# Kernel tuning notes

Measured on AMD Instinct MI355X. Metric: run time of the kernel, lower is better.

Reference implementation:

```python
import jax, jax.numpy as jnp
import numpy as np

D, H, N, BS = 3072, 2048, 16, 512
MAX_LATENT_VAR = 0.1


def setup_inputs() -> dict:
    key = jax.random.key(0)
    ks = jax.random.split(key, 12)
    s = 0.02
    return {
        "x": jax.random.normal(ks[0], (BS, D), dtype=jnp.float32),
        "eps": jax.random.normal(ks[1], (1, BS, N), dtype=jnp.float32),
        "enc_W1": jax.random.normal(ks[2], (D, H), dtype=jnp.float32) * s,
        "enc_b1": jnp.zeros((H,), dtype=jnp.float32),
        "enc_Wmu": jax.random.normal(ks[3], (H, N), dtype=jnp.float32) * s,
        "enc_bmu": jnp.zeros((N,), dtype=jnp.float32),
        "enc_Wls": jax.random.normal(ks[4], (H, 1), dtype=jnp.float32) * s,
        "enc_bls": jnp.zeros((1,), dtype=jnp.float32),
        "dec_W1": jax.random.normal(ks[5], (N, H), dtype=jnp.float32) * 0.1,
        "dec_b1": jnp.zeros((H,), dtype=jnp.float32),
        "dec_W2": jax.random.normal(ks[6], (H, D), dtype=jnp.float32) * s,
        "dec_b2": jnp.zeros((D,), dtype=jnp.float32),
    }


def reference(x, eps, enc_W1, enc_b1, enc_Wmu, enc_bmu, enc_Wls, enc_bls,
              dec_W1, dec_b1, dec_W2, dec_b2):
    bs, Dd = x.shape
    n = dec_W1.shape[0]

    def dec(z):  # smooth 2-layer MLP decoder (supports nested autodiff)
        return jnp.tanh(z @ dec_W1 + dec_b1) @ dec_W2 + dec_b2

    # encoder.forward_with_sigma
    h = jnp.tanh(x @ enc_W1 + enc_b1)
    z_star = h @ enc_Wmu + enc_bmu                      # (bs, n)
    sigma = jnp.exp(h @ enc_Wls + enc_bls)[:, 0]        # (bs,)

    # per-sample Jacobian of decoder: (bs, D, n)
    J = jax.vmap(jax.jacfwd(dec))(z_star)

    # per-sample Hessian of f(z) = stop_grad(d) . d,  d = (x - dec(z)) / sigma
    def f_hess(z, xi, sg):
        d = (xi - dec(z)) / sg
        return jnp.dot(jax.lax.stop_gradient(d), d)
    hess = jax.vmap(jax.hessian(f_hess), in_axes=(0, 0, 0))(z_star, x, sigma)  # (bs,n,n)

    eye = jnp.eye(n, dtype=x.dtype)
    Prec = jnp.einsum('bdi,bdj->bij', J, J) / (sigma ** 2)[:, None, None] + eye + hess

    eigvals = jnp.linalg.eigvalsh(Prec)                 # ascending, (bs, n)
    eigmin = eigvals[:, 0]
    delta = 1.0 / MAX_LATENT_VAR - eigmin               # (bs,)
    Prec = Prec + eye * delta[:, None, None]
    eigvals = eigvals + delta[:, None]

    # upper-triangular Cholesky: U^T U = Prec
    U = jnp.swapaxes(jnp.linalg.cholesky(Prec), -1, -2)  # (bs, n, n)

    def solve1(u, e):  # solve U y = e
        return jax.scipy.linalg.solve_triangular(u, e[:, None], lower=False)[:, 0]
    z_off = jax.vmap(jax.vmap(solve1, in_axes=(0, 0)), in_axes=(None, 0))(U, eps)  # (ne,bs,n)
    z_sample = z_star[None] + z_off

    n_eval = eps.shape[0]
    recon = dec(z_sample.reshape(-1, n)).reshape(n_eval, bs, Dd)
    recon_loss = ((recon - x[None]) ** 2).sum(axis=2).mean(axis=0) / (2.0 * sigma ** 2)
    latent_energy = (z_star ** 2).sum(axis=1) / 2.0 + (1.0 / eigvals).sum(axis=1) / 2.0
    logdet_loss = jnp.log(eigvals).sum(axis=1) / 2.0
    sigma_loss = Dd * jnp.log(sigma)
    neg_log_prob = (recon_loss + latent_energy + logdet_loss + sigma_loss) / Dd
    return (neg_log_prob, recon_loss, latent_energy, logdet_loss, sigma)
```

## Files before the change

### kernel.cpp

```cpp
#include <hip/hip_runtime.h>
#include <hip/hip_bf16.h>
#include <math.h>

#define D_ 3072
#define H_ 2048
#define N_ 16
#define BS_ 512

typedef short s16x8 __attribute__((ext_vector_type(8)));
typedef float f32x4v __attribute__((ext_vector_type(4)));
typedef __hip_bfloat16 bf16;

__device__ __forceinline__ void gload_lds16(const void* g, void* l) {
    __builtin_amdgcn_global_load_lds((const __attribute__((address_space(1))) void*)g,
                                     (__attribute__((address_space(3))) void*)l, 16, 0, 0);
}

__device__ __forceinline__ float bf2f(unsigned short u) {
    unsigned v = (unsigned)u << 16; float f; __builtin_memcpy(&f, &v, 4); return f;
}

__global__ __launch_bounds__(256) void mfma_nt_sk(
    const bf16* __restrict__ A, const bf16* __restrict__ Bt,
    float* __restrict__ C, int M, int N, int K, int KC)
{
    __shared__ __align__(16) bf16 As[128 * 32];
    __shared__ __align__(16) bf16 Bs[128 * 32];
    const int tid = threadIdx.x;
    const int w = tid >> 6, l = tid & 63;
    const int wr = w >> 1, wc = w & 1;
    const int m0 = blockIdx.y * 128, n0 = blockIdx.x * 128;
    const int kbeg = blockIdx.z * KC;

    f32x4v acc[4][4];
    #pragma unroll
    for (int a = 0; a < 4; ++a)
        #pragma unroll
        for (int b = 0; b < 4; ++b) acc[a][b] = (f32x4v){0.f, 0.f, 0.f, 0.f};

    const int srow = l >> 2;
    const int scol = (l & 3) * 8;

    for (int k0 = kbeg; k0 < kbeg + KC; k0 += 32) {
        #pragma unroll
        for (int q = 0; q < 2; ++q) {
            int r0 = w * 32 + q * 16;
            gload_lds16(&A[(size_t)(m0 + r0 + srow) * K + k0 + scol], &As[r0 * 32]);
            gload_lds16(&Bt[(size_t)(n0 + r0 + srow) * K + k0 + scol], &Bs[r0 * 32]);
        }
        __syncthreads();
        s16x8 af[4], bfr[4];
        #pragma unroll
        for (int mf = 0; mf < 4; ++mf)
            af[mf] = *(const s16x8*)&As[(wr * 64 + mf * 16 + (l & 15)) * 32 + (l >> 4) * 8];
        #pragma unroll
        for (int nf = 0; nf < 4; ++nf)
            bfr[nf] = *(const s16x8*)&Bs[(wc * 64 + nf * 16 + (l & 15)) * 32 + (l >> 4) * 8];
        #pragma unroll
        for (int mf = 0; mf < 4; ++mf)
            #pragma unroll
            for (int nf = 0; nf < 4; ++nf)
                acc[mf][nf] = __builtin_amdgcn_mfma_f32_16x16x32_bf16(af[mf], bfr[nf], acc[mf][nf], 0, 0, 0);
        __syncthreads();
    }

    #pragma unroll
    for (int mf = 0; mf < 4; ++mf)
        #pragma unroll
        for (int nf = 0; nf < 4; ++nf) {
            int n = n0 + wc * 64 + nf * 16 + (l & 15);
            #pragma unroll
            for (int r = 0; r < 4; ++r) {
                int m = m0 + wr * 64 + mf * 16 + (l >> 4) * 4 + r;
                atomicAdd(&C[(size_t)m * N + n], acc[mf][nf][r]);
            }
        }
}

__global__ __launch_bounds__(256) void ep_ebf(const float* __restrict__ C,
    const float* __restrict__ bias, const float* __restrict__ X,
    bf16* __restrict__ Eout, int MN, int N)
{
    int base = (blockIdx.x * 256 + threadIdx.x) * 8;
    if (base < MN) {
        float4 c0 = *(const float4*)&C[base];
        float4 c1 = *(const float4*)&C[base + 4];
        float4 x0 = *(const float4*)&X[base];
        float4 x1 = *(const float4*)&X[base + 4];
        int n = base % N;
        float4 b0 = *(const float4*)&bias[n];
        float4 b1 = *(const float4*)&bias[n + 4];
        union { s16x8 v; bf16 e[8]; } u;
        u.e[0] = __float2bfloat16(x0.x - (c0.x + b0.x));
        u.e[1] = __float2bfloat16(x0.y - (c0.y + b0.y));
        u.e[2] = __float2bfloat16(x0.z - (c0.z + b0.z));
        u.e[3] = __float2bfloat16(x0.w - (c0.w + b0.w));
        u.e[4] = __float2bfloat16(x1.x - (c1.x + b1.x));
        u.e[5] = __float2bfloat16(x1.y - (c1.y + b1.y));
        u.e[6] = __float2bfloat16(x1.z - (c1.z + b1.z));
        u.e[7] = __float2bfloat16(x1.w - (c1.w + b1.w));
        *(s16x8*)&Eout[base] = u.v;
    }
}

__global__ __launch_bounds__(256) void ep_recon(const float* __restrict__ C,
    const float* __restrict__ bias, const float* __restrict__ X, float* __restrict__ rls)
{
    int m = blockIdx.x;
    float s = 0.f;
    for (int n = threadIdx.x * 4; n < D_; n += 1024) {
        float4 c = *(const float4*)&C[(size_t)m * D_ + n];
        float4 bb = *(const float4*)&bias[n];
        float4 xx = *(const float4*)&X[(size_t)m * D_ + n];
        float v0 = c.x + bb.x - xx.x, v1 = c.y + bb.y - xx.y;
        float v2 = c.z + bb.z - xx.z, v3 = c.w + bb.w - xx.w;
        s += v0 * v0 + v1 * v1 + v2 * v2 + v3 * v3;
    }
    __shared__ float red[4];
    int wid = threadIdx.x >> 6, lane = threadIdx.x & 63;
    #pragma unroll
    for (int off = 32; off; off >>= 1) s += __shfl_xor(s, off);
    if (lane == 0) red[wid] = s;
    __syncthreads();
    if (threadIdx.x == 0) rls[m] = red[0] + red[1] + red[2] + red[3];
}

__global__ __launch_bounds__(256) void jtj_fused(
    const bf16* __restrict__ Vt, const bf16* __restrict__ W2t,
    float* __restrict__ S, int Mb, int b0)
{
    __shared__ union {
        struct { __align__(16) bf16 As[128 * 32]; __align__(16) bf16 Bs[128 * 32]; } s;
        __align__(16) bf16 J[128 * 136];
    } u;
    const int tid = threadIdx.x;
    const int w = tid >> 6, l = tid & 63;
    const int wr = w >> 1, wc = w & 1;

    int mb, nb;
    if ((Mb & 7) == 0) {
        int lin = blockIdx.y * 24 + blockIdx.x;
        int xcd = lin & 7, idx = lin >> 3;
        int mchunk = Mb >> 3;
        mb = xcd * mchunk + idx / 24;
        nb = idx % 24;
    } else { mb = blockIdx.y; nb = blockIdx.x; }
    const int m0 = mb * 128, n0 = nb * 128;

    f32x4v acc[4][4];
    #pragma unroll
    for (int a = 0; a < 4; ++a)
        #pragma unroll
        for (int b = 0; b < 4; ++b) acc[a][b] = (f32x4v){0.f, 0.f, 0.f, 0.f};

    const int srow = l >> 2;
    const int scol = (l & 3) * 8;

    for (int k0 = 0; k0 < H_; k0 += 32) {
        #pragma unroll
        for (int q = 0; q < 2; ++q) {
            int r0 = w * 32 + q * 16;
            gload_lds16(&Vt[(size_t)(m0 + r0 + srow) * H_ + k0 + scol], &u.s.As[r0 * 32]);
            gload_lds16(&W2t[(size_t)(n0 + r0 + srow) * H_ + k0 + scol], &u.s.Bs[r0 * 32]);
        }
        __syncthreads();
        s16x8 af[4], bfr[4];
        #pragma unroll
        for (int mf = 0; mf < 4; ++mf)
            af[mf] = *(const s16x8*)&u.s.As[(wr * 64 + mf * 16 + (l & 15)) * 32 + (l >> 4) * 8];
        #pragma unroll
        for (int nf = 0; nf < 4; ++nf)
            bfr[nf] = *(const s16x8*)&u.s.Bs[(wc * 64 + nf * 16 + (l & 15)) * 32 + (l >> 4) * 8];
        #pragma unroll
        for (int mf = 0; mf < 4; ++mf)
            #pragma unroll
            for (int nf = 0; nf < 4; ++nf)
                acc[mf][nf] = __builtin_amdgcn_mfma_f32_16x16x32_bf16(af[mf], bfr[nf], acc[mf][nf], 0, 0, 0);
        __syncthreads();
    }

    __syncthreads();
    #pragma unroll
    for (int mf = 0; mf < 4; ++mf) {
        int rbase = wr * 64 + mf * 16 + (l >> 4) * 4;
        #pragma unroll
        for (int nf = 0; nf < 4; ++nf) {
            int col = wc * 64 + nf * 16 + (l & 15);
            #pragma unroll
            for (int r = 0; r < 4; ++r)
                u.J[(rbase + r) * 136 + col] = __float2bfloat16(acc[mf][nf][r]);
        }
    }
    __syncthreads();

    #pragma unroll
    for (int t2 = 0; t2 < 2; ++t2) {
        int bl = w * 2 + t2;
        f32x4v sp = (f32x4v){0.f, 0.f, 0.f, 0.f};
        #pragma unroll
        for (int kq = 0; kq < 4; ++kq) {
            s16x8 fr = *(const s16x8*)&u.J[(bl * 16 + (l & 15)) * 136 + kq * 32 + (l >> 4) * 8];
            sp = __builtin_amdgcn_mfma_f32_16x16x32_bf16(fr, fr, sp, 0, 0, 0);
        }
        int bglob = b0 + mb * 8 + bl;
        #pragma unroll
        for (int r = 0; r < 4; ++r)
            atomicAdd(&S[(size_t)bglob * 256 + ((l >> 4) * 4 + r) * 16 + (l & 15)], sp[r]);
    }
}

__global__ __launch_bounds__(256) void hess_mfma(const float* __restrict__ t,
    const float* __restrict__ g, const bf16* __restrict__ W1b, float* __restrict__ S)
{
    const int w = threadIdx.x >> 6, l = threadIdx.x & 63;
    const int b = blockIdx.x * 4 + w;
    const int row = l & 15, kq = (l >> 4) * 8;

    f32x4v sp = (f32x4v){0.f, 0.f, 0.f, 0.f};
    for (int k0 = 0; k0 < H_; k0 += 32) {
        int kk = k0 + kq;
        s16x8 wf = *(const s16x8*)&W1b[(size_t)row * H_ + kk];
        float4 t0 = *(const float4*)&t[(size_t)b * H_ + kk];
        float4 t1 = *(const float4*)&t[(size_t)b * H_ + kk + 4];
        float4 g0 = *(const float4*)&g[(size_t)b * H_ + kk];
        float4 g1 = *(const float4*)&g[(size_t)b * H_ + kk + 4];
        float wv[8];
        wv[0] = 2.f * g0.x * t0.x * (1.f - t0.x * t0.x);
        wv[1] = 2.f * g0.y * t0.y * (1.f - t0.y * t0.y);
        wv[2] = 2.f * g0.z * t0.z * (1.f - t0.z * t0.z);
        wv[3] = 2.f * g0.w * t0.w * (1.f - t0.w * t0.w);
        wv[4] = 2.f * g1.x * t1.x * (1.f - t1.x * t1.x);
        wv[5] = 2.f * g1.y * t1.y * (1.f - t1.y * t1.y);
        wv[6] = 2.f * g1.z * t1.z * (1.f - t1.z * t1.z);
        wv[7] = 2.f * g1.w * t1.w * (1.f - t1.w * t1.w);
        union { s16x8 v; bf16 e[8]; } af;
        #pragma unroll
        for (int e = 0; e < 8; ++e)
            af.e[e] = __float2bfloat16(wv[e] * bf2f((unsigned short)wf[e]));
        sp = __builtin_amdgcn_mfma_f32_16x16x32_bf16(af.v, wf, sp, 0, 0, 0);
    }
    #pragma unroll
    for (int r = 0; r < 4; ++r)
        S[(size_t)b * 256 + ((l >> 4) * 4 + r) * 16 + (l & 15)] += sp[r];
}

__global__ __launch_bounds__(256) void prep_all(
    const float* __restrict__ x, const float* __restrict__ enc_W1,
    const float* __restrict__ dec_W2, const float* __restrict__ dec_W1,
    bf16* __restrict__ x_bf, bf16* __restrict__ eW1t,
    bf16* __restrict__ W2t, bf16* __restrict__ W2b, bf16* __restrict__ W1b)
{
    __shared__ float tile[64][65];
    const int blk = blockIdx.x;
    const int tid = threadIdx.x;
    if (blk < 768) {
        int i = blk * 256 + tid;
        const float4* p = (const float4*)x + (size_t)i * 2;
        float4 a = p[0], b = p[1];
        union { s16x8 v; bf16 e[8]; } u;
        u.e[0] = __float2bfloat16(a.x); u.e[1] = __float2bfloat16(a.y);
        u.e[2] = __float2bfloat16(a.z); u.e[3] = __float2bfloat16(a.w);
        u.e[4] = __float2bfloat16(b.x); u.e[5] = __float2bfloat16(b.y);
        u.e[6] = __float2bfloat16(b.z); u.e[7] = __float2bfloat16(b.w);
        *(s16x8*)&x_bf[(size_t)i * 8] = u.v;
    } else if (blk < 768 + 1536) {
        int bid = blk - 768;
        int r0 = (bid % 48) * 64, c0 = (bid / 48) * 64;
        int tx = tid & 63, ty = tid >> 6;
        #pragma unroll
        for (int k = 0; k < 16; ++k) {
            int rr = ty * 16 + k;
            tile[rr][tx] = enc_W1[(size_t)(r0 + rr) * H_ + c0 + tx];
        }
        __syncthreads();
        #pragma unroll
        for (int k = 0; k < 16; ++k) {
            int cc = ty * 16 + k;
            eW1t[(size_t)(c0 + cc) * D_ + r0 + tx] = __float2bfloat16(tile[tx][cc]);
        }
    } else if (blk < 768 + 3072) {
        int bid = blk - 768 - 1536;
        int r0 = (bid % 32) * 64, c0 = (bid / 32) * 64;
        int tx = tid & 63, ty = tid >> 6;
        #pragma unroll
        for (int k = 0; k < 16; ++k) {
            int rr = ty * 16 + k;
            float v = dec_W2[(size_t)(r0 + rr) * D_ + c0 + tx];
            tile[rr][tx] = v;
            W2b[(size_t)(r0 + rr) * D_ + c0 + tx] = __float2bfloat16(v);
        }
        __syncthreads();
        #pragma unroll
        for (int k = 0; k < 16; ++k) {
            int cc = ty * 16 + k;
            W2t[(size_t)(c0 + cc) * H_ + r0 + tx] = __float2bfloat16(tile[tx][cc]);
        }
    } else {
        int i = (blk - 768 - 3072) * 256 + tid;
        if (i < N_ * H_ / 8) {
            const float4* p = (const float4*)dec_W1 + (size_t)i * 2;
            float4 a = p[0], b = p[1];
            union { s16x8 v; bf16 e[8]; } u;
            u.e[0] = __float2bfloat16(a.x); u.e[1] = __float2bfloat16(a.y);
            u.e[2] = __float2bfloat16(a.z); u.e[3] = __float2bfloat16(a.w);
            u.e[4] = __float2bfloat16(b.x); u.e[5] = __float2bfloat16(b.y);
            u.e[6] = __float2bfloat16(b.z); u.e[7] = __float2bfloat16(b.w);
            *(s16x8*)&W1b[(size_t)i * 8] = u.v;
        }
    }
}

__global__ __launch_bounds__(256) void zsig_t_kernel(const float* __restrict__ Ch,
    const float* __restrict__ enc_b1, const float* __restrict__ Wmu, const float* __restrict__ bmu,
    const float* __restrict__ Wls, const float* __restrict__ bls,
    const float* __restrict__ dW1, const float* __restrict__ db1,
    float* __restrict__ z_star, float* __restrict__ lsig, float* __restrict__ sigma,
    float* __restrict__ t, bf16* __restrict__ tb)
{
    const int b = blockIdx.x, tid = threadIdx.x;
    float acc[17];
    #pragma unroll
    for (int i = 0; i < 17; ++i) acc[i] = 0.f;
    for (int hh = tid; hh < H_; hh += 256) {
        float hv = tanhf(Ch[(size_t)b * H_ + hh] + enc_b1[hh]);
        const float* wr = &Wmu[(size_t)hh * 16];
        #pragma unroll
        for (int i = 0; i < 16; ++i) acc[i] += hv * wr[i];
        acc[16] += hv * Wls[hh];
    }
    __shared__ float red[17][4];
    __shared__ float zs[16];
    const int wid = tid >> 6, lane = tid & 63;
    #pragma unroll
    for (int i = 0; i < 17; ++i) {
        float v = acc[i];
        #pragma unroll
        for (int off = 32; off; off >>= 1) v += __shfl_xor(v, off);
        if (lane == 0) red[i][wid] = v;
    }
    __syncthreads();
    if (tid < 17) {
        float v = red[tid][0] + red[tid][1] + red[tid][2] + red[tid][3];
        if (tid < 16) { float z = v + bmu[tid]; zs[tid] = z; z_star[(size_t)b * 16 + tid] = z; }
        else { float ls = v + bls[0]; lsig[b] = ls; sigma[b] = expf(ls); }
    }
    __syncthreads();
    for (int hh = tid; hh < H_; hh += 256) {
        float a = db1[hh];
        #pragma unroll
        for (int i = 0; i < 16; ++i) a += zs[i] * dW1[(size_t)i * H_ + hh];
        float tv = tanhf(a);
        t[(size_t)b * H_ + hh] = tv;
        tb[(size_t)b * H_ + hh] = __float2bfloat16(tv);
    }
}

__global__ __launch_bounds__(256) void build_t(const float* __restrict__ z,
    const float* __restrict__ W1, const float* __restrict__ b1, bf16* __restrict__ tb)
{
    __shared__ float zs[16];
    int b = blockIdx.x, tid = threadIdx.x;
    if (tid < 16) zs[tid] = z[(size_t)b * 16 + tid];
    __syncthreads();
    for (int hh = tid; hh < H_; hh += 256) {
        float a = b1[hh];
        #pragma unroll
        for (int i = 0; i < 16; ++i) a += zs[i] * W1[(size_t)i * H_ + hh];
        tb[(size_t)b * H_ + hh] = __float2bfloat16(tanhf(a));
    }
}

__global__ __launch_bounds__(256) void build_vt(const float* __restrict__ t,
    const float* __restrict__ W1, bf16* __restrict__ Vt, int b0)
{
    int bl = blockIdx.x, b = b0 + bl, tid = threadIdx.x;
    __shared__ float u[H_];
    for (int hh = tid; hh < H_; hh += 256) {
        float tv = t[(size_t)b * H_ + hh];
        u[hh] = 1.f - tv * tv;
    }
    __syncthreads();
    size_t base = (size_t)bl * 16 * H_;
    int hh = tid * 8;
    for (int i = 0; i < 16; ++i) {
        union { s16x8 v; bf16 e[8]; } pk;
        #pragma unroll
        for (int k = 0; k < 8; ++k)
            pk.e[k] = __float2bfloat16(u[hh + k] * W1[(size_t)i * H_ + hh + k]);
        *(s16x8*)&Vt[base + (size_t)i * H_ + hh] = pk.v;
    }
}

__global__ __launch_bounds__(64) void solve_kernel(const float* __restrict__ S,
    const float* __restrict__ sigma, const float* __restrict__ z_star,
    const float* __restrict__ eps, float* __restrict__ z_sample, float* __restrict__ d_out)
{
    const int lane = threadIdx.x;
    const int q = lane >> 4;
    const int j = lane & 15;
    const int b = blockIdx.x * 4 + q;

    const float sg = sigma[b];
    const float inv_s2 = 1.0f / (sg * sg);

    float a0[16], a[16];
    #pragma unroll
    for (int r = 0; r < 16; ++r) {
        a0[r] = S[(size_t)b * 256 + r * 16 + j] * inv_s2 + ((r == j) ? 1.0f : 0.0f);
        a[r] = a0[r];
    }

    #pragma unroll
    for (int k = 0; k < 14; ++k) {
        float x[16];
        #pragma unroll
        for (int r = 0; r < 16; ++r) x[r] = __shfl(a[k], r, 16);
        float sig2 = 0.f;
        #pragma unroll
        for (int r = 0; r < 16; ++r) if (r > k + 1) sig2 += x[r] * x[r];
        float x0 = x[k + 1];
        float normx = sqrtf(sig2 + x0 * x0);
        float alpha = (x0 >= 0.f) ? -normx : normx;
        float v[16];
        #pragma unroll
        for (int r = 0; r < 16; ++r)
            v[r] = (r <= k) ? 0.f : ((r == k + 1) ? x0 - alpha : x[r]);
        float vtv = 0.f;
        #pragma unroll
        for (int r = 0; r < 16; ++r) vtv += v[r] * v[r];
        float beta = (vtv > 1e-28f) ? 2.0f / vtv : 0.f;
        float sj = 0.f;
        #pragma unroll
        for (int r = 0; r < 16; ++r) sj += a[r] * v[r];
        float av[16];
        #pragma unroll
        for (int r = 0; r < 16; ++r) av[r] = __shfl(sj, r, 16);
        float vtav = 0.f;
        #pragma unroll
        for (int r = 0; r < 16; ++r) vtav += v[r] * av[r];
        float c = 0.5f * beta * vtav;
        float wv[16];
        #pragma unroll
        for (int r = 0; r < 16; ++r) wv[r] = beta * (av[r] - c * v[r]);
        float vj = (j <= k) ? 0.f : ((j == k + 1) ? a[k] - alpha : a[k]);
        float wj = beta * (sj - c * vj);
        #pragma unroll
        for (int r = 0; r < 16; ++r) a[r] -= v[r] * wj + wv[r] * vj;
    }

    float dg[16], eo[15];
    #pragma unroll
    for (int r = 0; r < 16; ++r) dg[r] = __shfl(a[r], r, 16);
    #pragma unroll
    for (int r = 0; r < 15; ++r) eo[r] = __shfl(a[r + 1], r, 16);

    float lo = 1e30f, hi = 1e30f;
    #pragma unroll
    for (int r = 0; r < 16; ++r) {
        float rad = ((r > 0) ? fabsf(eo[r - 1]) : 0.f) + ((r < 15) ? fabsf(eo[r]) : 0.f);
        lo = fminf(lo, dg[r] - rad);
        hi = fminf(hi, dg[r]);
    }
    lo -= 1e-4f; hi += 1e-4f;

    #pragma unroll
    for (int pass = 0; pass < 5; ++pass) {
        float step = (hi - lo) * (1.0f / 17.0f);
        float s = lo + step * (float)(j + 1);
        float qq = dg[0] - s;
        int cnt = (qq < 0.f) ? 1 : 0;
        #pragma unroll
        for (int i = 1; i < 16; ++i) {
            float denom = (fabsf(qq) < 1e-30f) ? -1e-30f : qq;
            qq = dg[i] - s - eo[i - 1] * eo[i - 1] / denom;
            cnt += (qq < 0.f) ? 1 : 0;
        }
        unsigned long long bal = __ballot(cnt >= 1);
        unsigned grp = (unsigned)((bal >> (q * 16)) & 0xffffull);
        int f = grp ? (__ffs(grp) - 1) : 16;
        float nlo = lo + step * (float)f;
        float nhi = (f < 16) ? (lo + step * (float)(f + 1)) : hi;
        lo = nlo; hi = nhi;
    }
    const float lam_min = 0.5f * (lo + hi);
    const float delta = 10.0f - lam_min;

    float bm[16];
    #pragma unroll
    for (int r = 0; r < 16; ++r) bm[r] = a0[r] + ((r == j) ? delta : 0.f);

    float ldsum = 0.f;
    #pragma unroll
    for (int kk = 0; kk < 16; ++kk) {
        float ck[16];
        #pragma unroll
        for (int r = 0; r < 16; ++r) ck[r] = __shfl(bm[kk], r, 16);
        float dkk = sqrtf(fmaxf(ck[kk], 1e-30f));
        float inv = 1.0f / dkk;
        ldsum += logf(dkk);
        float lfull[16];
        #pragma unroll
        for (int r = 0; r < 16; ++r) lfull[r] = ck[r] * inv;
        float lj = bm[kk] * inv;
        if (j == kk) {
            #pragma unroll
            for (int r = 0; r < 16; ++r) bm[r] = (r >= kk) ? lfull[r] : 0.f;
        } else if (j > kk) {
            #pragma unroll
            for (int r = 0; r < 16; ++r)
                if (r > kk) bm[r] -= lfull[r] * lj;
        }
    }

    float w[16];
    #pragma unroll
    for (int r = 0; r < 16; ++r) w[r] = 0.f;
    #pragma unroll
    for (int i = 0; i < 16; ++i) {
        float row[16];
        #pragma unroll
        for (int kx = 0; kx < 16; ++kx) row[kx] = __shfl(bm[i], kx, 16);
        float sacc = 0.f;
        #pragma unroll
        for (int kx = 0; kx < 16; ++kx) if (kx < i) sacc += row[kx] * w[kx];
        float invd = 1.0f / row[i];
        float val = (i == j) ? invd : (-sacc * invd);
        w[i] = (i >= j) ? val : 0.f;
    }

    float tsum = 0.f;
    #pragma unroll
    for (int r = 0; r < 16; ++r) tsum += w[r] * w[r];
    float zv = z_star[(size_t)b * 16 + j];
    float ep = eps[(size_t)b * 16 + j];
    float epsv[16];
    #pragma unroll
    for (int r = 0; r < 16; ++r) epsv[r] = __shfl(ep, r, 16);
    float zoff = 0.f;
    #pragma unroll
    for (int r = 0; r < 16; ++r) zoff += w[r] * epsv[r];
    z_sample[(size_t)b * 16 + j] = zv + zoff;

    float zsq = zv * zv;
    #pragma unroll
    for (int off = 1; off < 16; off <<= 1) {
        tsum += __shfl_xor(tsum, off);
        zsq  += __shfl_xor(zsq, off);
    }
    if (j == 0) {
        d_out[2 * 512 + b] = 0.5f * zsq + 0.5f * tsum;
        d_out[3 * 512 + b] = ldsum;
        d_out[4 * 512 + b] = sg;
    }
}

__global__ void finalize_kernel(const float* __restrict__ rlsum, const float* __restrict__ sigma,
    const float* __restrict__ lsig, float* __restrict__ d_out)
{
    int b = blockIdx.x * 256 + threadIdx.x;
    if (b < BS_) {
        float sg = sigma[b];
        float rl = rlsum[b] / (2.0f * sg * sg);
        float le = d_out[2 * 512 + b];
        float ld = d_out[3 * 512 + b];
        d_out[b] = (rl + le + ld) / 3072.0f + lsig[b];
        d_out[512 + b] = rl;
    }
}

extern "C" void kernel_launch(void* const* d_in, const int* in_sizes, int n_in,
                              void* d_out, int out_size, void* d_ws, size_t ws_size,
                              hipStream_t stream)
{
    const float* x       = (const float*)d_in[0];
    const float* eps     = (const float*)d_in[1];
    const float* enc_W1  = (const float*)d_in[2];
    const float* enc_b1  = (const float*)d_in[3];
    const float* enc_Wmu = (const float*)d_in[4];
    const float* enc_bmu = (const float*)d_in[5];
    const float* enc_Wls = (const float*)d_in[6];
    const float* enc_bls = (const float*)d_in[7];
    const float* dec_W1  = (const float*)d_in[8];
    const float* dec_b1  = (const float*)d_in[9];
    const float* dec_W2  = (const float*)d_in[10];
    const float* dec_b2  = (const float*)d_in[11];
    float* out = (float*)d_out;

    char* wsb = (char*)d_ws;
    size_t off = 0;
    auto alloc = [&](size_t bytes) -> void* {
        off = (off + 255) & ~(size_t)255;
        void* p = wsb + off;
        off += bytes;
        return p;
    };

    float* Ch   = (float*)alloc((size_t)BS_ * H_ * 4);
    float* Cd   = (float*)alloc((size_t)BS_ * D_ * 4);
    float* g    = (float*)alloc((size_t)BS_ * H_ * 4);
    float* S    = (float*)alloc((size_t)BS_ * 256 * 4);
    size_t zero_span = (size_t)((char*)(S + BS_ * 256) - (char*)Ch);

    float* t    = (float*)alloc((size_t)BS_ * H_ * 4);
    float* z_st = (float*)alloc((size_t)BS_ * 16 * 4);
    float* lsig = (float*)alloc(BS_ * 4);
    float* sigm = (float*)alloc(BS_ * 4);
    float* z_sm = (float*)alloc((size_t)BS_ * 16 * 4);
    float* rls  = (float*)alloc(BS_ * 4);
    bf16* x_bf  = (bf16*)alloc((size_t)BS_ * D_ * 2);
    bf16* eW1t  = (bf16*)alloc((size_t)H_ * D_ * 2);
    bf16* W2b   = (bf16*)alloc((size_t)H_ * D_ * 2);
    bf16* W2t   = (bf16*)alloc((size_t)D_ * H_ * 2);
    bf16* W1b   = (bf16*)alloc((size_t)N_ * H_ * 2);
    bf16* t_bf  = (bf16*)alloc((size_t)BS_ * H_ * 2);
    bf16* e_bf  = (bf16*)alloc((size_t)BS_ * D_ * 2);
    bf16* t2b   = (bf16*)alloc((size_t)BS_ * H_ * 2);

    int nb = 0;
    size_t base_off = off;
    const int cand[3] = {512, 128, 32};
    bf16* Vt = nullptr;
    for (int ci = 0; ci < 3; ++ci) {
        off = base_off;
        int n = cand[ci];
        bf16* vt = (bf16*)alloc((size_t)n * 16 * H_ * 2);
        if (off <= ws_size) { nb = n; Vt = vt; break; }
    }
    if (nb == 0) return;

    prep_all<<<dim3(768 + 3072 + 16), 256, 0, stream>>>(
        x, enc_W1, dec_W2, dec_W1, x_bf, eW1t, W2t, W2b, W1b);
    hipMemsetAsync(Ch, 0, zero_span, stream);

    mfma_nt_sk<<<dim3(H_ / 128, BS_ / 128, 4), 256, 0, stream>>>(
        x_bf, eW1t, Ch, BS_, H_, D_, D_ / 4);
    zsig_t_kernel<<<dim3(BS_), 256, 0, stream>>>(Ch, enc_b1, enc_Wmu, enc_bmu, enc_Wls, enc_bls,
        dec_W1, dec_b1, z_st, lsig, sigm, t, t_bf);
    mfma_nt_sk<<<dim3(D_ / 128, BS_ / 128, 4), 256, 0, stream>>>(
        t_bf, W2t, Cd, BS_, D_, H_, H_ / 4);
    ep_ebf<<<dim3(BS_ * D_ / 8 / 256), 256, 0, stream>>>(Cd, dec_b2, x, e_bf, BS_ * D_, D_);
    mfma_nt_sk<<<dim3(H_ / 128, BS_ / 128, 4), 256, 0, stream>>>(
        e_bf, W2b, g, BS_, H_, D_, D_ / 4);

    for (int b0 = 0; b0 < BS_; b0 += nb) {
        build_vt<<<dim3(nb), 256, 0, stream>>>(t, dec_W1, Vt, b0);
        jtj_fused<<<dim3(D_ / 128, nb * 16 / 128), 256, 0, stream>>>(
            Vt, W2t, S, nb * 16 / 128, b0);
    }
    hess_mfma<<<dim3(BS_ / 4), 256, 0, stream>>>(t, g, W1b, S);

    solve_kernel<<<dim3(BS_ / 4), 64, 0, stream>>>(S, sigm, z_st, eps, z_sm, out);
    build_t<<<dim3(BS_), 256, 0, stream>>>(z_sm, dec_W1, dec_b1, t2b);
    hipMemsetAsync(Cd, 0, (size_t)BS_ * D_ * 4, stream);
    mfma_nt_sk<<<dim3(D_ / 128, BS_ / 128, 4), 256, 0, stream>>>(
        t2b, W2t, Cd, BS_, D_, H_, H_ / 4);
    ep_recon<<<dim3(BS_), 256, 0, stream>>>(Cd, dec_b2, x, rls);
    finalize_kernel<<<dim3(2), 256, 0, stream>>>(rls, sigm, lsig, out);
}
```

Before: 359.3 us.

## Rewrite JtJ GEMM as 256x256-tile, 8-wave double-buffered MFMA kernel

Replaces the 128x128 jtj_fused kernel with jtj8: 512-thread blocks computing 256x256 tiles over 64-wide K steps. Shared-memory staging is double-buffered with XOR-swizzled LDS layout, and prefetch is interleaved with the MFMA phases using barriers and setprio. It also uses an XCD-aware block swizzle and a two-pass epilogue that builds the per-sample J^T J. The aim is more data reuse per global load, fewer bank conflicts and overlap of loads with compute. In exchange it needs 128 KB of dynamic LDS with one block per CU, and it assumes nb*16 is a multiple of 256 and the block count a multiple of 8.

Result: slower. 386.2 us (+7.5%).

```diff
diff --git a/kernel.cpp b/kernel.cpp
--- a/kernel.cpp
+++ b/kernel.cpp
@@ -6,6 +6,7 @@
 #define H_ 2048
 #define N_ 16
 #define BS_ 512
+#define NT_ (H_ / 64)
 
 typedef short s16x8 __attribute__((ext_vector_type(8)));
 typedef float f32x4v __attribute__((ext_vector_type(4)));
@@ -125,87 +126,124 @@
     if (threadIdx.x == 0) rls[m] = red[0] + red[1] + red[2] + red[3];
 }
 
-__global__ __launch_bounds__(256) void jtj_fused(
+__global__ __launch_bounds__(512, 1) void jtj8(
     const bf16* __restrict__ Vt, const bf16* __restrict__ W2t,
-    float* __restrict__ S, int Mb, int b0)
-{
-    __shared__ union {
-        struct { __align__(16) bf16 As[128 * 32]; __align__(16) bf16 Bs[128 * 32]; } s;
-        __align__(16) bf16 J[128 * 136];
-    } u;
+    float* __restrict__ S, int nwg, int b0)
+{
+    extern __shared__ __align__(16) char smem[];
+    char* Abase = smem;
+    char* Bbase = smem + 65536;
     const int tid = threadIdx.x;
     const int w = tid >> 6, l = tid & 63;
-    const int wr = w >> 1, wc = w & 1;
-
-    int mb, nb;
-    if ((Mb & 7) == 0) {
-        int lin = blockIdx.y * 24 + blockIdx.x;
-        int xcd = lin & 7, idx = lin >> 3;
-        int mchunk = Mb >> 3;
-        mb = xcd * mchunk + idx / 24;
-        nb = idx % 24;
-    } else { mb = blockIdx.y; nb = blockIdx.x; }
-    const int m0 = mb * 128, n0 = nb * 128;
-
-    f32x4v acc[4][4];
-    #pragma unroll
-    for (int a = 0; a < 4; ++a)
-        #pragma unroll
-        for (int b = 0; b < 4; ++b) acc[a][b] = (f32x4v){0.f, 0.f, 0.f, 0.f};
-
-    const int srow = l >> 2;
-    const int scol = (l & 3) * 8;
-
-    for (int k0 = 0; k0 < H_; k0 += 32) {
-        #pragma unroll
-        for (int q = 0; q < 2; ++q) {
-            int r0 = w * 32 + q * 16;
-            gload_lds16(&Vt[(size_t)(m0 + r0 + srow) * H_ + k0 + scol], &u.s.As[r0 * 32]);
-            gload_lds16(&W2t[(size_t)(n0 + r0 + srow) * H_ + k0 + scol], &u.s.Bs[r0 * 32]);
+    const int wr = w >> 2, wc = w & 3;
+
+    const int bid = blockIdx.x;
+    const int swz = (bid & 7) * (nwg >> 3) + (bid >> 3);
+    const int mb = swz / 12, nbk = swz % 12;
+    const int m0 = mb * 256, n0 = nbk * 256;
+
+    const int srow = tid >> 3;
+    const int sswz = (((tid & 7) ^ ((tid >> 3) & 7)) << 4);
+
+    f32x4v acc[8][4];
+    #pragma unroll
+    for (int i = 0; i < 8; ++i)
+        #pragma unroll
+        for (int j = 0; j < 4; ++j) acc[i][j] = (f32x4v){0.f, 0.f, 0.f, 0.f};
+
+    auto STAGE = [&](int u, int t, int bi) {
+        const char* gsrc;
+        char* ldst;
+        if (u < 2) {
+            gsrc = (const char*)Vt + ((size_t)(m0 + u * 128 + srow) * H_ + t * 64) * 2 + sswz;
+            ldst = Abase + bi * 32768 + u * 16384 + w * 1024;
+        } else {
+            gsrc = (const char*)W2t + ((size_t)(n0 + (u - 2) * 128 + srow) * H_ + t * 64) * 2 + sswz;
+            ldst = Bbase + bi * 32768 + (u - 2) * 16384 + w * 1024;
+        }
+        gload_lds16(gsrc, ldst);
+        gload_lds16(gsrc + (size_t)64 * H_ * 2, ldst + 8192);
+    };
+
+    #pragma unroll
+    for (int u = 0; u < 4; ++u) STAGE(u, 0, 0);
+    asm volatile("s_waitcnt vmcnt(0)" ::: "memory");
+    __builtin_amdgcn_s_barrier();
+    __builtin_amdgcn_sched_barrier(0);
+
+    for (int T = 0; T < NT_; ++T) {
+        const int bi = T & 1;
+        const char* Ab = Abase + bi * 32768;
+        const char* Bb = Bbase + bi * 32768;
+        #pragma unroll
+        for (int p = 0; p < 4; ++p) {
+            const int qa = p >> 1, qb = p & 1;
+            s16x8 af[4][2], bfv[2][2];
+            #pragma unroll
+            for (int i = 0; i < 4; ++i) {
+                int arow = wr * 128 + (qa * 4 + i) * 16 + (l & 15);
+                #pragma unroll
+                for (int kh = 0; kh < 2; ++kh)
+                    af[i][kh] = *(const s16x8*)(Ab + arow * 128 +
+                        ((kh * 64 + (l >> 4) * 16) ^ ((l & 7) << 4)));
+            }
+            #pragma unroll
+            for (int j = 0; j < 2; ++j) {
+                int brow = wc * 64 + (qb * 2 + j) * 16 + (l & 15);
+                #pragma unroll
+                for (int kh = 0; kh < 2; ++kh)
+                    bfv[j][kh] = *(const s16x8*)(Bb + brow * 128 +
+                        ((kh * 64 + (l >> 4) * 16) ^ ((l & 7) << 4)));
+            }
+            if (T + 1 < NT_) STAGE(p, T + 1, bi ^ 1);
+            if (p == 3) asm volatile("s_waitcnt vmcnt(0)" ::: "memory");
+            __builtin_amdgcn_s_barrier();
+            __builtin_amdgcn_sched_barrier(0);
+            __builtin_amdgcn_s_setprio(1);
+            #pragma unroll
+            for (int i = 0; i < 4; ++i)
+                #pragma unroll
+                for (int j = 0; j < 2; ++j) {
+                    acc[qa * 4 + i][qb * 2 + j] = __builtin_amdgcn_mfma_f32_16x16x32_bf16(
+                        af[i][0], bfv[j][0], acc[qa * 4 + i][qb * 2 + j], 0, 0, 0);
+                    acc[qa * 4 + i][qb * 2 + j] = __builtin_amdgcn_mfma_f32_16x16x32_bf16(
+                        af[i][1], bfv[j][1], acc[qa * 4 + i][qb * 2 + j], 0, 0, 0);
+                }
+            __builtin_amdgcn_s_setprio(0);
+            __builtin_amdgcn_s_barrier();
+            __builtin_amdgcn_sched_barrier(0);
+        }
+    }
+
+    __syncthreads();
+    bf16* Jl = (bf16*)smem;
+    const int bbase = b0 + mb * 16;
+    #pragma unroll
+    for (int h = 0; h < 2; ++h) {
+        if (wr == h) {
+            #pragma unroll
+            for (int mf = 0; mf < 8; ++mf)
+                #pragma unroll
+                for (int nf = 0; nf < 4; ++nf) {
+                    int rowb = mf * 16 + (l >> 4) * 4;
+                    int col = wc * 64 + nf * 16 + (l & 15);
+                    #pragma unroll
+                    for (int r = 0; r < 4; ++r)
+                        Jl[(rowb + r) * 264 + col] = __float2bfloat16(acc[mf][nf][r]);
+                }
         }
         __syncthreads();
-        s16x8 af[4], bfr[4];
-        #pragma unroll
-        for (int mf = 0; mf < 4; ++mf)
-            af[mf] = *(const s16x8*)&u.s.As[(wr * 64 + mf * 16 + (l & 15)) * 32 + (l >> 4) * 8];
-        #pragma unroll
-        for (int nf = 0; nf < 4; ++nf)
-            bfr[nf] = *(const s16x8*)&u.s.Bs[(wc * 64 + nf * 16 + (l & 15)) * 32 + (l >> 4) * 8];
-        #pragma unroll
-        for (int mf = 0; mf < 4; ++mf)
-            #pragma unroll
-            for (int nf = 0; nf < 4; ++nf)
-                acc[mf][nf] = __builtin_amdgcn_mfma_f32_16x16x32_bf16(af[mf], bfr[nf], acc[mf][nf], 0, 0, 0);
+        f32x4v sp = (f32x4v){0.f, 0.f, 0.f, 0.f};
+        #pragma unroll
+        for (int kq = 0; kq < 8; ++kq) {
+            s16x8 fr = *(const s16x8*)&Jl[((size_t)w * 16 + (l & 15)) * 264 + kq * 32 + (l >> 4) * 8];
+            sp = __builtin_amdgcn_mfma_f32_16x16x32_bf16(fr, fr, sp, 0, 0, 0);
+        }
+        int bg = bbase + h * 8 + w;
+        #pragma unroll
+        for (int r = 0; r < 4; ++r)
+            atomicAdd(&S[(size_t)bg * 256 + ((l >> 4) * 4 + r) * 16 + (l & 15)], sp[r]);
         __syncthreads();
-    }
-
-    __syncthreads();
-    #pragma unroll
-    for (int mf = 0; mf < 4; ++mf) {
-        int rbase = wr * 64 + mf * 16 + (l >> 4) * 4;
-        #pragma unroll
-        for (int nf = 0; nf < 4; ++nf) {
-            int col = wc * 64 + nf * 16 + (l & 15);
-            #pragma unroll
-            for (int r = 0; r < 4; ++r)
-                u.J[(rbase + r) * 136 + col] = __float2bfloat16(acc[mf][nf][r]);
-        }
-    }
-    __syncthreads();
-
-    #pragma unroll
-    for (int t2 = 0; t2 < 2; ++t2) {
-        int bl = w * 2 + t2;
-        f32x4v sp = (f32x4v){0.f, 0.f, 0.f, 0.f};
-        #pragma unroll
-        for (int kq = 0; kq < 4; ++kq) {
-            s16x8 fr = *(const s16x8*)&u.J[(bl * 16 + (l & 15)) * 136 + kq * 32 + (l >> 4) * 8];
-            sp = __builtin_amdgcn_mfma_f32_16x16x32_bf16(fr, fr, sp, 0, 0, 0);
-        }
-        int bglob = b0 + mb * 8 + bl;
-        #pragma unroll
-        for (int r = 0; r < 4; ++r)
-            atomicAdd(&S[(size_t)bglob * 256 + ((l >> 4) * 4 + r) * 16 + (l & 15)], sp[r]);
     }
 }
 
@@ -644,8 +682,8 @@
 
     for (int b0 = 0; b0 < BS_; b0 += nb) {
         build_vt<<<dim3(nb), 256, 0, stream>>>(t, dec_W1, Vt, b0);
-        jtj_fused<<<dim3(D_ / 128, nb * 16 / 128), 256, 0, stream>>>(
-            Vt, W2t, S, nb * 16 / 128, b0);
+        int Mb = nb * 16 / 256;
+        jtj8<<<dim3(Mb * 12), 512, 131072, stream>>>(Vt, W2t, S, Mb * 12, b0);
     }
     hess_mfma<<<dim3(BS_ / 4), 256, 0, stream>>>(t, g, W1b, S);
 
```

## Triple-buffer jtj_fused K loop with XOR-swizzled LDS and single barrier

Applied to the files above, without the earlier changes.

Replaces the single-buffered K loop in the jtj_fused GEMM with a 3-stage LDS ring. Global-to-LDS loads are issued two tiles ahead and waited on with explicit vmcnt counts, and the loop uses one barrier per iteration instead of two. It also XOR-swizzles the 16-byte chunks in LDS to cut bank conflicts on the fragment reads. This triples the A/B staging LDS (still within the union with the J tile) and relies on hand-counted waitcnt values being correct.

Result: no change. 359.5 us (+0.1%).

```diff
diff --git a/kernel.cpp b/kernel.cpp
--- a/kernel.cpp
+++ b/kernel.cpp
@@ -130,22 +130,22 @@
     float* __restrict__ S, int Mb, int b0)
 {
     __shared__ union {
-        struct { __align__(16) bf16 As[128 * 32]; __align__(16) bf16 Bs[128 * 32]; } s;
+        struct { __align__(16) bf16 As[3][128 * 32]; __align__(16) bf16 Bs[3][128 * 32]; } s;
         __align__(16) bf16 J[128 * 136];
     } u;
     const int tid = threadIdx.x;
     const int w = tid >> 6, l = tid & 63;
     const int wr = w >> 1, wc = w & 1;
 
-    int mb, nb;
+    int mb, nbk;
     if ((Mb & 7) == 0) {
         int lin = blockIdx.y * 24 + blockIdx.x;
         int xcd = lin & 7, idx = lin >> 3;
         int mchunk = Mb >> 3;
         mb = xcd * mchunk + idx / 24;
-        nb = idx % 24;
-    } else { mb = blockIdx.y; nb = blockIdx.x; }
-    const int m0 = mb * 128, n0 = nb * 128;
+        nbk = idx % 24;
+    } else { mb = blockIdx.y; nbk = blockIdx.x; }
+    const int m0 = mb * 128, n0 = nbk * 128;
 
     f32x4v acc[4][4];
     #pragma unroll
@@ -153,30 +153,47 @@
         #pragma unroll
         for (int b = 0; b < 4; ++b) acc[a][b] = (f32x4v){0.f, 0.f, 0.f, 0.f};
 
-    const int srow = l >> 2;
-    const int scol = (l & 3) * 8;
-
-    for (int k0 = 0; k0 < H_; k0 += 32) {
-        #pragma unroll
-        for (int q = 0; q < 2; ++q) {
-            int r0 = w * 32 + q * 16;
-            gload_lds16(&Vt[(size_t)(m0 + r0 + srow) * H_ + k0 + scol], &u.s.As[r0 * 32]);
-            gload_lds16(&W2t[(size_t)(n0 + r0 + srow) * H_ + k0 + scol], &u.s.Bs[r0 * 32]);
-        }
-        __syncthreads();
+    const int strow = tid >> 2;
+    const int scb = (((tid & 3) ^ ((tid >> 3) & 3)) << 4);
+
+    auto STAGE = [&](int kt, int bi) {
+        const char* a0 = (const char*)Vt  + ((size_t)(m0 + strow) * H_ + kt * 32) * 2 + scb;
+        const char* b0p = (const char*)W2t + ((size_t)(n0 + strow) * H_ + kt * 32) * 2 + scb;
+        char* la = (char*)u.s.As[bi] + w * 1024;
+        char* lb = (char*)u.s.Bs[bi] + w * 1024;
+        gload_lds16(a0, la);
+        gload_lds16(a0 + (size_t)64 * H_ * 2, la + 4096);
+        gload_lds16(b0p, lb);
+        gload_lds16(b0p + (size_t)64 * H_ * 2, lb + 4096);
+    };
+
+    STAGE(0, 0);
+    STAGE(1, 1);
+
+    const int rdcb = (((l >> 4) ^ ((l >> 1) & 3)) << 4);
+
+    for (int kt = 0; kt < H_ / 32; ++kt) {
+        __builtin_amdgcn_sched_barrier(0);
+        if (kt == H_ / 32 - 1) asm volatile("s_waitcnt vmcnt(0)" ::: "memory");
+        else                   asm volatile("s_waitcnt vmcnt(4)" ::: "memory");
+        __builtin_amdgcn_s_barrier();
+        __builtin_amdgcn_sched_barrier(0);
+        const int cur = kt % 3;
+        const char* Ab = (const char*)u.s.As[cur];
+        const char* Bb = (const char*)u.s.Bs[cur];
         s16x8 af[4], bfr[4];
         #pragma unroll
         for (int mf = 0; mf < 4; ++mf)
-            af[mf] = *(const s16x8*)&u.s.As[(wr * 64 + mf * 16 + (l & 15)) * 32 + (l >> 4) * 8];
+            af[mf] = *(const s16x8*)(Ab + (wr * 64 + mf * 16 + (l & 15)) * 64 + rdcb);
         #pragma unroll
         for (int nf = 0; nf < 4; ++nf)
-            bfr[nf] = *(const s16x8*)&u.s.Bs[(wc * 64 + nf * 16 + (l & 15)) * 32 + (l >> 4) * 8];
+            bfr[nf] = *(const s16x8*)(Bb + (wc * 64 + nf * 16 + (l & 15)) * 64 + rdcb);
+        if (kt + 2 < H_ / 32) STAGE(kt + 2, (kt + 2) % 3);
         #pragma unroll
         for (int mf = 0; mf < 4; ++mf)
             #pragma unroll
             for (int nf = 0; nf < 4; ++nf)
                 acc[mf][nf] = __builtin_amdgcn_mfma_f32_16x16x32_bf16(af[mf], bfr[nf], acc[mf][nf], 0, 0, 0);
-        __syncthreads();
     }
 
     __syncthreads();
```
